# Kernel optimization log

Measured on AMD Instinct MI355X. Metric: run time of the kernel, lower is better.

Reference implementation:

```python
import jax, jax.numpy as jnp
import numpy as np
import math

NUM_HEADS = 16
THETA = 10000.0


def _rope(x, token_pos, theta):
    # x: [B, H, S, d_k]; token_pos: [S]
    d_k = x.shape[-1]
    freqs = 1.0 / theta ** (jnp.arange(0, d_k, 2, dtype=jnp.float32) / d_k)  # [d_k/2]
    angles = token_pos.astype(jnp.float32)[:, None] * freqs[None, :]         # [S, d_k/2]
    cos, sin = jnp.cos(angles), jnp.sin(angles)
    x1 = x[..., 0::2]
    x2 = x[..., 1::2]
    out1 = x1 * cos - x2 * sin
    out2 = x1 * sin + x2 * cos
    # interleave back: (..., d_k/2, 2) -> (..., d_k)
    return jnp.stack([out1, out2], axis=-1).reshape(x.shape)


def setup_inputs() -> dict:
    key = jax.random.key(0)
    ks = jax.random.split(key, 5)
    B, S, D = 4, 2048, 1024
    scale = 0.02
    return {
        "x": jax.random.normal(ks[0], (B, S, D), dtype=jnp.float32),
        "token_pos": jnp.arange(S, dtype=jnp.int64 if jax.config.jax_enable_x64 else jnp.int32),
        "Wq": jax.random.normal(ks[1], (D, D), dtype=jnp.float32) * scale,
        "Wk": jax.random.normal(ks[2], (D, D), dtype=jnp.float32) * scale,
        "Wv": jax.random.normal(ks[3], (D, D), dtype=jnp.float32) * scale,
        "Wo": jax.random.normal(ks[4], (D, D), dtype=jnp.float32) * scale,
    }


def reference(x, token_pos, Wq, Wk, Wv, Wo):
    B, S, D = x.shape
    H = NUM_HEADS
    d_k = D // H
    # projections (Linear without bias: y = x @ W^T, W is [out, in])
    def proj(W):
        y = jnp.einsum('bsd,ed->bse', x, W)
        return y.reshape(B, S, H, d_k).transpose(0, 2, 1, 3)  # [B,H,S,d_k]
    q, k, v = proj(Wq), proj(Wk), proj(Wv)
    q = _rope(q, token_pos, THETA)
    k = _rope(k, token_pos, THETA)
    scores = jnp.einsum('bhqd,bhkd->bhqk', q, k) / math.sqrt(d_k)
    causal = jnp.tril(jnp.ones((S, S), dtype=bool))
    scores = jnp.where(causal, scores, -jnp.inf)
    attn = jax.nn.softmax(scores, axis=-1)
    out = jnp.einsum('bhqk,bhkd->bhqd', attn, v)            # [B,H,S,d_k]
    out = out.transpose(0, 2, 1, 3).reshape(B, S, D)
    return jnp.einsum('bsd,ed->bse', out, Wo)
```

## Files before the change

### kernel.cpp

```cpp
#include <hip/hip_runtime.h>

typedef unsigned short u16;
typedef __bf16 bf16x8 __attribute__((ext_vector_type(8)));
typedef float f32x4 __attribute__((ext_vector_type(4)));
typedef u16 u16x8 __attribute__((ext_vector_type(8)));

#define B_ 4
#define S_ 2048
#define D_ 1024
#define H_ 16
#define LOG2E 1.44269504f

__device__ inline u16 f2bf(float f) {
  unsigned u = __float_as_uint(f);
  u = u + 0x7fffu + ((u >> 16) & 1u);
  return (u16)(u >> 16);
}
__device__ inline u16 f2bf_hw(float f) {
  __bf16 b = (__bf16)f;
  return __builtin_bit_cast(u16, b);
}
__device__ inline float bf2f(u16 h) {
  return __uint_as_float(((unsigned)h) << 16);
}
__device__ inline void gload_lds16(const u16* g, u16* l) {
  __builtin_amdgcn_global_load_lds((const __attribute__((address_space(1))) void*)g,
                                   (__attribute__((address_space(3))) void*)l, 16, 0, 0);
}

__global__ __launch_bounds__(256) void k_f32_to_bf16(const float* __restrict__ src,
                                                     u16* __restrict__ dst, int n4) {
  int i = blockIdx.x * 256 + threadIdx.x;
  if (i >= n4) return;
  float4 v = reinterpret_cast<const float4*>(src)[i];
  ushort4 o;
  o.x = f2bf(v.x); o.y = f2bf(v.y); o.z = f2bf(v.z); o.w = f2bf(v.w);
  reinterpret_cast<ushort4*>(dst)[i] = o;
}

__global__ __launch_bounds__(256) void k_cvt_w4(const float* __restrict__ w0,
                                                const float* __restrict__ w1,
                                                const float* __restrict__ w2,
                                                const float* __restrict__ w3,
                                                u16* __restrict__ dst) {
  int i = blockIdx.x * 256 + threadIdx.x;
  const int tensor = i >> 18;
  const int local = i & 262143;
  const float* s = tensor == 0 ? w0 : tensor == 1 ? w1 : tensor == 2 ? w2 : w3;
  float4 v = reinterpret_cast<const float4*>(s)[local];
  ushort4 o;
  o.x = f2bf(v.x); o.y = f2bf(v.y); o.z = f2bf(v.z); o.w = f2bf(v.w);
  reinterpret_cast<ushort4*>(dst + (size_t)tensor * 1048576)[local] = o;
}

__global__ __launch_bounds__(256) void k_rope_table(const int* __restrict__ pos,
                                                    float2* __restrict__ tab) {
  int idx = blockIdx.x * 256 + threadIdx.x;
  if (idx >= S_ * 32) return;
  int s = idx >> 5, i = idx & 31;
  float freq = powf(10000.0f, -(float)i * (1.0f / 32.0f));
  float ang = (float)pos[s] * freq;
  float sn, c;
  sincosf(ang, &sn, &c);
  tab[idx] = make_float2(c, sn);
}

__global__ __launch_bounds__(256) void k_rope_k(u16* __restrict__ kb,
                                                const float2* __restrict__ tab) {
  int idx = blockIdx.x * 256 + threadIdx.x;
  const int row = idx >> 7;
  const int s = row & 2047;
  const int chunk = idx & 127;
  u16* p = kb + ((size_t)row << 10) + chunk * 8;
  u16x8 v = *reinterpret_cast<u16x8*>(p);
  const float4* tp = reinterpret_cast<const float4*>(tab + s * 32 + (chunk & 7) * 4);
  float4 t0 = tp[0], t1 = tp[1];
  float cc[4] = {t0.x, t0.z, t1.x, t1.z};
  float ss[4] = {t0.y, t0.w, t1.y, t1.w};
  u16x8 o;
#pragma unroll
  for (int u = 0; u < 4; u++) {
    float x1 = bf2f(v[2 * u]), x2 = bf2f(v[2 * u + 1]);
    o[2 * u]     = f2bf(x1 * cc[u] - x2 * ss[u]);
    o[2 * u + 1] = f2bf(x1 * ss[u] + x2 * cc[u]);
  }
  *reinterpret_cast<u16x8*>(p) = o;
}

__global__ __launch_bounds__(256) void k_gemm_qkv(const u16* __restrict__ A,
                                                  const u16* __restrict__ Bcat,
                                                  u16* __restrict__ Ccat) {
  __shared__ u16 As[128 * 64];
  __shared__ u16 Bs[128 * 64];
  const int K = 1024;
  const int swz = (blockIdx.x & 7) * 192 + (blockIdx.x >> 3);
  const int bx = swz % 24;
  const int by = swz / 24;
  const int m0 = by << 7, n0 = bx << 7;
  const int tid = threadIdx.x;
  const int lane = tid & 63;
  const int wv = tid >> 6;
  const int wm = (wv >> 1) << 6;
  const int wn = (wv & 1) << 6;
  const int r = lane & 15, g = lane >> 4;

  f32x4 acc[4][4] = {};

  const int srow0 = tid >> 3;
  const int scol = (((tid & 7) ^ ((tid >> 3) & 7)) * 8);
  const int csw = r & 7;

  for (int k0 = 0; k0 < K; k0 += 64) {
#pragma unroll
    for (int i = 0; i < 4; i++)
      gload_lds16(A + (size_t)(m0 + srow0 + 32 * i) * K + k0 + scol,
                  As + tid * 8 + i * 2048);
#pragma unroll
    for (int i = 0; i < 4; i++)
      gload_lds16(Bcat + (size_t)(n0 + srow0 + 32 * i) * K + k0 + scol,
                  Bs + tid * 8 + i * 2048);
    __syncthreads();
#pragma unroll
    for (int ks = 0; ks < 2; ks++) {
      bf16x8 af[4], bfr[4];
#pragma unroll
      for (int i = 0; i < 4; i++)
        af[i] = *reinterpret_cast<const bf16x8*>(
            &As[(wm + i * 16 + r) * 64 + (((ks * 4 + g) ^ csw) * 8)]);
#pragma unroll
      for (int t = 0; t < 4; t++)
        bfr[t] = *reinterpret_cast<const bf16x8*>(
            &Bs[(wn + t * 16 + r) * 64 + (((ks * 4 + g) ^ csw) * 8)]);
#pragma unroll
      for (int i = 0; i < 4; i++)
#pragma unroll
        for (int t = 0; t < 4; t++)
          acc[i][t] = __builtin_amdgcn_mfma_f32_16x16x32_bf16(af[i], bfr[t], acc[i][t], 0, 0, 0);
    }
    __syncthreads();
  }

  u16* Cb = Ccat + (size_t)(n0 >> 10) * (8192 * 1024);
  const int c0 = n0 & 1023;
#pragma unroll
  for (int i = 0; i < 4; i++) {
#pragma unroll
    for (int t = 0; t < 4; t++) {
      const int row = m0 + wm + i * 16 + g * 4;
      const int col = c0 + wn + t * 16 + r;
#pragma unroll
      for (int j = 0; j < 4; j++)
        Cb[(size_t)(row + j) * 1024 + col] = f2bf(acc[i][t][j]);
    }
  }
}

__global__ __launch_bounds__(256) void k_gemm_bt(const u16* __restrict__ A,
                                                 const u16* __restrict__ Bw,
                                                 float* __restrict__ C,
                                                 int M, int N, int K) {
  __shared__ u16 As[128 * 64];
  __shared__ u16 Bs[128 * 64];
  const int nbx = N >> 7;
  const int swz = (blockIdx.x & 7) * (gridDim.x >> 3) + (blockIdx.x >> 3);
  const int bx = swz % nbx;
  const int by = swz / nbx;
  const int m0 = by << 7, n0 = bx << 7;
  const int tid = threadIdx.x;
  const int lane = tid & 63;
  const int wv = tid >> 6;
  const int wm = (wv >> 1) << 6;
  const int wn = (wv & 1) << 6;
  const int r = lane & 15, g = lane >> 4;

  f32x4 acc[4][4] = {};

  const int srow0 = tid >> 3;
  const int scol = (((tid & 7) ^ ((tid >> 3) & 7)) * 8);
  const int csw = r & 7;

  for (int k0 = 0; k0 < K; k0 += 64) {
#pragma unroll
    for (int i = 0; i < 4; i++)
      gload_lds16(A + (size_t)(m0 + srow0 + 32 * i) * K + k0 + scol,
                  As + tid * 8 + i * 2048);
#pragma unroll
    for (int i = 0; i < 4; i++)
      gload_lds16(Bw + (size_t)(n0 + srow0 + 32 * i) * K + k0 + scol,
                  Bs + tid * 8 + i * 2048);
    __syncthreads();
#pragma unroll
    for (int ks = 0; ks < 2; ks++) {
      bf16x8 af[4], bfr[4];
#pragma unroll
      for (int i = 0; i < 4; i++)
        af[i] = *reinterpret_cast<const bf16x8*>(
            &As[(wm + i * 16 + r) * 64 + (((ks * 4 + g) ^ csw) * 8)]);
#pragma unroll
      for (int t = 0; t < 4; t++)
        bfr[t] = *reinterpret_cast<const bf16x8*>(
            &Bs[(wn + t * 16 + r) * 64 + (((ks * 4 + g) ^ csw) * 8)]);
#pragma unroll
      for (int i = 0; i < 4; i++)
#pragma unroll
        for (int t = 0; t < 4; t++)
          acc[i][t] = __builtin_amdgcn_mfma_f32_16x16x32_bf16(af[i], bfr[t], acc[i][t], 0, 0, 0);
    }
    __syncthreads();
  }

#pragma unroll
  for (int i = 0; i < 4; i++) {
#pragma unroll
    for (int t = 0; t < 4; t++) {
      const int row = m0 + wm + i * 16 + g * 4;
      const int col = n0 + wn + t * 16 + r;
#pragma unroll
      for (int j = 0; j < 4; j++)
        C[(size_t)(row + j) * N + col] = acc[i][t][j];
    }
  }
}

__global__ __launch_bounds__(256) void k_transpose_v(const u16* __restrict__ Vb,
                                                     u16* __restrict__ Vt) {
  __shared__ u16 tile[64][65];
  int bh = blockIdx.x >> 5;
  int st = blockIdx.x & 31;
  int b = bh >> 4, h = bh & 15;
  int s0 = st << 6;
  int tid = threadIdx.x;
#pragma unroll
  for (int rr = 0; rr < 16; rr++) {
    int idx = rr * 256 + tid;
    int sl = idx >> 6, d = idx & 63;
    tile[d][sl] = Vb[(size_t)(b * S_ + s0 + sl) * 1024 + h * 64 + d];
  }
  __syncthreads();
#pragma unroll
  for (int rr = 0; rr < 16; rr++) {
    int idx = rr * 256 + tid;
    int d = idx >> 6, sl = idx & 63;
    Vt[(size_t)(bh * 64 + d) * 2048 + s0 + sl] = tile[d][sl];
  }
}

__global__ __launch_bounds__(256) void k_attn12(const u16* __restrict__ Q,
                                                const u16* __restrict__ Kb,
                                                const u16* __restrict__ Vt,
                                                const float2* __restrict__ tab,
                                                u16* __restrict__ O) {
  __shared__ u16 Ks[64 * 64];
  __shared__ u16 Vs[64 * 64];
  __shared__ u16 Ps[4][32 * 64];

  const int bh = (blockIdx.x & 7) * 8 + ((blockIdx.x >> 3) & 7);
  const int qt = 15 - (blockIdx.x >> 6);
  const int b = bh >> 4, h = bh & 15;
  const int tid = threadIdx.x;
  const int lane = tid & 63, w = tid >> 6;
  const int g = lane >> 4, r = lane & 15;

  const u16* Kbase = Kb + (size_t)(b * S_) * 1024 + h * 64;
  const u16* Vbase = Vt + (size_t)bh * 64 * 2048;

  const int srow = tid >> 3;
  const int scol = ((tid & 7) * 8) ^ ((srow & 7) * 8);
  const int rsw = (r & 7) * 8;

  const int qbase = qt << 7;
  const int qrow0 = qbase + (w << 5);

  const float QSC = 0.125f * LOG2E;
  bf16x8 qf[2][2];
#pragma unroll
  for (int f = 0; f < 2; f++) {
    const int s = qrow0 + f * 16 + r;
    const u16* qrow = Q + (size_t)(b * S_ + s) * 1024 + h * 64;
    qf[f][0] = *reinterpret_cast<const bf16x8*>(qrow + g * 8);
    qf[f][1] = *reinterpret_cast<const bf16x8*>(qrow + 32 + g * 8);
    const float4* tp = reinterpret_cast<const float4*>(tab + s * 32);
#pragma unroll
    for (int c = 0; c < 2; c++) {
      float4 t0 = tp[c * 8 + g * 2], t1 = tp[c * 8 + g * 2 + 1];
      float cc[4] = {t0.x, t0.z, t1.x, t1.z};
      float ss[4] = {t0.y, t0.w, t1.y, t1.w};
      bf16x8 q = qf[f][c];
#pragma unroll
      for (int u = 0; u < 4; u++) {
        float x1 = (float)q[2 * u], x2 = (float)q[2 * u + 1];
        q[2 * u]     = (__bf16)((x1 * cc[u] - x2 * ss[u]) * QSC);
        q[2 * u + 1] = (__bf16)((x1 * ss[u] + x2 * cc[u]) * QSC);
      }
      qf[f][c] = q;
    }
  }

  f32x4 o_acc[2][4] = {};
  float l0 = 0.f, l1 = 0.f;
  u16* pb0 = &Ps[w][r * 64];
  u16* pb1 = &Ps[w][(16 + r) * 64];

  const u16* kp0 = Kbase + (size_t)srow * 1024 + scol;
  const u16* kp1 = kp0 + 32 * 1024;
  const u16* vp0 = Vbase + (size_t)srow * 2048 + scol;
  const u16* vp1 = vp0 + 32 * 2048;

  const int kend = qbase + 128;
  for (int k0 = 0; k0 < kend; k0 += 64) {
    gload_lds16(kp0, Ks + tid * 8);
    gload_lds16(kp1, Ks + tid * 8 + 2048);
    gload_lds16(vp0, Vs + tid * 8);
    gload_lds16(vp1, Vs + tid * 8 + 2048);
    kp0 += 64 * 1024; kp1 += 64 * 1024; vp0 += 64; vp1 += 64;
    __syncthreads();

    if (k0 <= qrow0 + 31) {
      const int rem0 = qrow0 + 15 - k0;
      const int rem1 = qrow0 + 31 - k0;
      const int ktlim0 = rem0 < 0 ? 0 : (rem0 >= 48 ? 4 : (rem0 >> 4) + 1);
      const int ktlim1 = rem1 >= 48 ? 4 : (rem1 >> 4) + 1;
      const bool mask0 = (k0 + 63 > qrow0);
      const bool mask1 = (k0 + 63 > qrow0 + 16);

#pragma unroll
      for (int kt = 0; kt < 4; kt++) {
        const int pc = (kt * 16 + g * 4) ^ rsw;
        if (kt >= ktlim1) {
          ushort4 z = {0, 0, 0, 0};
          *reinterpret_cast<ushort4*>(pb0 + pc) = z;
          *reinterpret_cast<ushort4*>(pb1 + pc) = z;
          continue;
        }
        const int krow = kt * 16 + r;
        bf16x8 kf0 = *reinterpret_cast<const bf16x8*>(&Ks[krow * 64 + ((g * 8) ^ rsw)]);
        bf16x8 kf1 = *reinterpret_cast<const bf16x8*>(&Ks[krow * 64 + ((32 + g * 8) ^ rsw)]);
        f32x4 s0 = {}, s1 = {};
        if (kt < ktlim0) {
          s0 = __builtin_amdgcn_mfma_f32_16x16x32_bf16(kf0, qf[0][0], s0, 0, 0, 0);
          s0 = __builtin_amdgcn_mfma_f32_16x16x32_bf16(kf1, qf[0][1], s0, 0, 0, 0);
        }
        s1 = __builtin_amdgcn_mfma_f32_16x16x32_bf16(kf0, qf[1][0], s1, 0, 0, 0);
        s1 = __builtin_amdgcn_mfma_f32_16x16x32_bf16(kf1, qf[1][1], s1, 0, 0, 0);

        const int colb = k0 + kt * 16 + g * 4;
        float p0[4], p1[4];
        if (kt < ktlim0) {
          if (mask0) {
#pragma unroll
            for (int j = 0; j < 4; j++)
              if (colb + j > qrow0 + r) s0[j] = -1e30f;
          }
#pragma unroll
          for (int j = 0; j < 4; j++) p0[j] = exp2f(s0[j]);
          l0 += (p0[0] + p0[1]) + (p0[2] + p0[3]);
        } else {
#pragma unroll
          for (int j = 0; j < 4; j++) p0[j] = 0.f;
        }
        if (mask1) {
#pragma unroll
          for (int j = 0; j < 4; j++)
            if (colb + j > qrow0 + 16 + r) s1[j] = -1e30f;
        }
#pragma unroll
        for (int j = 0; j < 4; j++) p1[j] = exp2f(s1[j]);
        l1 += (p1[0] + p1[1]) + (p1[2] + p1[3]);

        ushort4 w0, w1;
        w0.x = f2bf_hw(p0[0]); w0.y = f2bf_hw(p0[1]); w0.z = f2bf_hw(p0[2]); w0.w = f2bf_hw(p0[3]);
        w1.x = f2bf_hw(p1[0]); w1.y = f2bf_hw(p1[1]); w1.z = f2bf_hw(p1[2]); w1.w = f2bf_hw(p1[3]);
        *reinterpret_cast<ushort4*>(pb0 + pc) = w0;
        *reinterpret_cast<ushort4*>(pb1 + pc) = w1;
      }
      asm volatile("s_waitcnt lgkmcnt(0)" ::: "memory");

#pragma unroll
      for (int kc = 0; kc < 2; kc++) {
        const int cb = (kc * 32 + g * 8) ^ rsw;
        bf16x8 pf0 = *reinterpret_cast<const bf16x8*>(pb0 + cb);
        bf16x8 pf1 = *reinterpret_cast<const bf16x8*>(pb1 + cb);
#pragma unroll
        for (int dt = 0; dt < 4; dt++) {
          bf16x8 vf = *reinterpret_cast<const bf16x8*>(
              &Vs[(dt * 16 + r) * 64 + ((kc * 32 + g * 8) ^ rsw)]);
          o_acc[0][dt] = __builtin_amdgcn_mfma_f32_16x16x32_bf16(pf0, vf, o_acc[0][dt], 0, 0, 0);
          o_acc[1][dt] = __builtin_amdgcn_mfma_f32_16x16x32_bf16(pf1, vf, o_acc[1][dt], 0, 0, 0);
        }
      }
    }
    __syncthreads();
  }

  l0 += __shfl_xor(l0, 16); l0 += __shfl_xor(l0, 32);
  l1 += __shfl_xor(l1, 16); l1 += __shfl_xor(l1, 32);

#pragma unroll
  for (int f = 0; f < 2; f++) {
    u16* orow = O + (size_t)(b * S_ + qrow0 + f * 16) * 1024 + h * 64;
#pragma unroll
    for (int j = 0; j < 4; j++) {
      const float ln = __shfl(f ? l1 : l0, 4 * g + j);
      const float rln = 1.0f / ln;
#pragma unroll
      for (int dt = 0; dt < 4; dt++)
        orow[(size_t)(g * 4 + j) * 1024 + dt * 16 + r] = f2bf(o_acc[f][dt][j] * rln);
    }
  }
}

extern "C" void kernel_launch(void* const* d_in, const int* in_sizes, int n_in,
                              void* d_out, int out_size, void* d_ws, size_t ws_size,
                              hipStream_t stream) {
  const float* x  = (const float*)d_in[0];
  const int*   pos = (const int*)d_in[1];
  const float* Wq = (const float*)d_in[2];
  const float* Wk = (const float*)d_in[3];
  const float* Wv = (const float*)d_in[4];
  const float* Wo = (const float*)d_in[5];
  float* out = (float*)d_out;

  char* ws = (char*)d_ws;
  size_t off = 0;
  auto alloc = [&](size_t bytes) {
    void* p = ws + off;
    off += (bytes + 255) & ~(size_t)255;
    return p;
  };
  const size_t XB = (size_t)8192 * 1024 * 2;
  u16* xb  = (u16*)alloc(XB);
  u16* wqb = (u16*)alloc((size_t)1024 * 1024 * 2);
  u16* wkb = (u16*)alloc((size_t)1024 * 1024 * 2);
  u16* wvb = (u16*)alloc((size_t)1024 * 1024 * 2);
  u16* wob = (u16*)alloc((size_t)1024 * 1024 * 2);
  u16* qb  = (u16*)alloc(XB);
  u16* kb  = (u16*)alloc(XB);
  u16* vb  = (u16*)alloc(XB);
  u16* vt  = (u16*)alloc(XB);
  float2* tab = (float2*)alloc((size_t)2048 * 32 * sizeof(float2));
  u16* ob = vb;
  (void)wkb; (void)wvb;

  k_f32_to_bf16<<<8192, 256, 0, stream>>>(x, xb, 2097152);
  k_cvt_w4<<<4096, 256, 0, stream>>>(Wq, Wk, Wv, Wo, wqb);
  k_rope_table<<<256, 256, 0, stream>>>(pos, tab);

  k_gemm_qkv<<<1536, 256, 0, stream>>>(xb, wqb, qb);

  k_rope_k<<<4096, 256, 0, stream>>>(kb, tab);

  k_transpose_v<<<2048, 256, 0, stream>>>(vb, vt);

  k_attn12<<<1024, 256, 0, stream>>>(qb, kb, vt, tab, ob);

  k_gemm_bt<<<512, 256, 0, stream>>>(ob, wob, out, 8192, 1024, 1024);
}
```

Measured before the change: 191.5 us.

## Double-buffer QKV GEMM with 256x128 tiles and 8-wave blocks

Replaces the QKV projection GEMM with a 512-thread, 256x128-tile variant. It double-buffers the LDS tiles, prefetching the next K slice while the current one is computed, and synchronises with explicit vmcnt waits and raw barriers. It also remaps blocks to XCDs so that each XCD owns a contiguous M range. The costs are more LDS per block (96KB) and tighter occupancy, and the waitcnt accounting has to exactly match the number of issued loads.

Result: no change. 194.7 us (+1.7%).

```diff
diff --git a/kernel.cpp b/kernel.cpp
--- a/kernel.cpp
+++ b/kernel.cpp
@@ -87,70 +87,90 @@
   *reinterpret_cast<u16x8*>(p) = o;
 }
 
-__global__ __launch_bounds__(256) void k_gemm_qkv(const u16* __restrict__ A,
-                                                  const u16* __restrict__ Bcat,
-                                                  u16* __restrict__ Ccat) {
-  __shared__ u16 As[128 * 64];
-  __shared__ u16 Bs[128 * 64];
+__global__ __launch_bounds__(512, 2) void k_gemm_qkv8(const u16* __restrict__ A,
+                                                      const u16* __restrict__ Bcat,
+                                                      u16* __restrict__ Ccat) {
+  __shared__ u16 Asl[2][2][128 * 64];
+  __shared__ u16 Bsl[2][128 * 64];
   const int K = 1024;
-  const int swz = (blockIdx.x & 7) * 192 + (blockIdx.x >> 3);
-  const int bx = swz % 24;
-  const int by = swz / 24;
-  const int m0 = by << 7, n0 = bx << 7;
+  const int bid = blockIdx.x;
+  const int xcd = bid & 7, idx = bid >> 3;
+  const int mp = xcd * 4 + idx / 24;
+  const int np = idx % 24;
+  const int m0 = mp << 8, n0 = np << 7;
   const int tid = threadIdx.x;
-  const int lane = tid & 63;
-  const int wv = tid >> 6;
-  const int wm = (wv >> 1) << 6;
-  const int wn = (wv & 1) << 6;
+  const int lane = tid & 63, w = tid >> 6;
+  const int wr = w >> 1, wc = w & 1;
   const int r = lane & 15, g = lane >> 4;
 
   f32x4 acc[4][4] = {};
 
-  const int srow0 = tid >> 3;
-  const int scol = (((tid & 7) ^ ((tid >> 3) & 7)) * 8);
+  const int srow = tid >> 3;
+  const int sch = ((tid & 7) ^ (srow & 7)) * 8;
   const int csw = r & 7;
 
-  for (int k0 = 0; k0 < K; k0 += 64) {
-#pragma unroll
-    for (int i = 0; i < 4; i++)
-      gload_lds16(A + (size_t)(m0 + srow0 + 32 * i) * K + k0 + scol,
-                  As + tid * 8 + i * 2048);
-#pragma unroll
-    for (int i = 0; i < 4; i++)
-      gload_lds16(Bcat + (size_t)(n0 + srow0 + 32 * i) * K + k0 + scol,
-                  Bs + tid * 8 + i * 2048);
-    __syncthreads();
-#pragma unroll
-    for (int ks = 0; ks < 2; ks++) {
+  const u16* Ab = A + (size_t)(m0 + srow) * K + sch;
+  const u16* Bb = Bcat + (size_t)(n0 + srow) * K + sch;
+
+#define STAGE(kt, bf) do {                                                   \
+    const u16* a_ = Ab + (size_t)(kt) * 64;                                  \
+    const u16* b_ = Bb + (size_t)(kt) * 64;                                  \
+    gload_lds16(a_,                   &Asl[bf][0][0] + tid * 8);             \
+    gload_lds16(a_ + (size_t)64 * K,  &Asl[bf][0][0] + tid * 8 + 4096);      \
+    gload_lds16(a_ + (size_t)128 * K, &Asl[bf][1][0] + tid * 8);             \
+    gload_lds16(a_ + (size_t)192 * K, &Asl[bf][1][0] + tid * 8 + 4096);      \
+    gload_lds16(b_,                   &Bsl[bf][0] + tid * 8);                \
+    gload_lds16(b_ + (size_t)64 * K,  &Bsl[bf][0] + tid * 8 + 4096);         \
+  } while (0)
+
+  STAGE(0, 0);
+
+  for (int t = 0; t < 16; ++t) {
+    const int b = t & 1;
+    if (t < 15) {
+      STAGE(t + 1, b ^ 1);
+      asm volatile("s_waitcnt vmcnt(6)" ::: "memory");
+    } else {
+      asm volatile("s_waitcnt vmcnt(0)" ::: "memory");
+    }
+    __builtin_amdgcn_s_barrier();
+    asm volatile("" ::: "memory");
+
+    const u16* Ah = &Asl[b][wr >> 1][0] + ((wr & 1) * 64) * 64;
+    const u16* Bh = &Bsl[b][0] + (wc * 64) * 64;
+#pragma unroll
+    for (int ks = 0; ks < 2; ++ks) {
       bf16x8 af[4], bfr[4];
 #pragma unroll
       for (int i = 0; i < 4; i++)
         af[i] = *reinterpret_cast<const bf16x8*>(
-            &As[(wm + i * 16 + r) * 64 + (((ks * 4 + g) ^ csw) * 8)]);
-#pragma unroll
-      for (int t = 0; t < 4; t++)
-        bfr[t] = *reinterpret_cast<const bf16x8*>(
-            &Bs[(wn + t * 16 + r) * 64 + (((ks * 4 + g) ^ csw) * 8)]);
+            &Ah[(i * 16 + r) * 64 + (((ks * 4 + g) ^ csw) * 8)]);
+#pragma unroll
+      for (int t2 = 0; t2 < 4; t2++)
+        bfr[t2] = *reinterpret_cast<const bf16x8*>(
+            &Bh[(t2 * 16 + r) * 64 + (((ks * 4 + g) ^ csw) * 8)]);
 #pragma unroll
       for (int i = 0; i < 4; i++)
 #pragma unroll
-        for (int t = 0; t < 4; t++)
-          acc[i][t] = __builtin_amdgcn_mfma_f32_16x16x32_bf16(af[i], bfr[t], acc[i][t], 0, 0, 0);
-    }
-    __syncthreads();
-  }
-
-  u16* Cb = Ccat + (size_t)(n0 >> 10) * (8192 * 1024);
+        for (int t2 = 0; t2 < 4; t2++)
+          acc[i][t2] = __builtin_amdgcn_mfma_f32_16x16x32_bf16(af[i], bfr[t2], acc[i][t2], 0, 0, 0);
+    }
+    asm volatile("" ::: "memory");
+    __builtin_amdgcn_s_barrier();
+  }
+#undef STAGE
+
+  u16* Cb = Ccat + (size_t)((n0) >> 10) * (8192 * 1024);
   const int c0 = n0 & 1023;
 #pragma unroll
   for (int i = 0; i < 4; i++) {
 #pragma unroll
-    for (int t = 0; t < 4; t++) {
-      const int row = m0 + wm + i * 16 + g * 4;
-      const int col = c0 + wn + t * 16 + r;
+    for (int t2 = 0; t2 < 4; t2++) {
+      const int row = m0 + wr * 64 + i * 16 + g * 4;
+      const int col = c0 + wc * 64 + t2 * 16 + r;
 #pragma unroll
       for (int j = 0; j < 4; j++)
-        Cb[(size_t)(row + j) * 1024 + col] = f2bf(acc[i][t][j]);
+        Cb[(size_t)(row + j) * 1024 + col] = f2bf(acc[i][t2][j]);
     }
   }
 }
@@ -445,7 +465,7 @@
   k_cvt_w4<<<4096, 256, 0, stream>>>(Wq, Wk, Wv, Wo, wqb);
   k_rope_table<<<256, 256, 0, stream>>>(pos, tab);
 
-  k_gemm_qkv<<<1536, 256, 0, stream>>>(xb, wqb, qb);
+  k_gemm_qkv8<<<768, 512, 0, stream>>>(xb, wqb, qb);
 
   k_rope_k<<<4096, 256, 0, stream>>>(kb, tab);
 
```
